# Kernel tuning notes

Measured on AMD Instinct MI355X. Metric: run time of the kernel, lower is better.

Reference implementation:

```python
import jax, jax.numpy as jnp
import numpy as np

K = 3       # kernel_size
STRIDE = 1
PAD = 1


def setup_inputs() -> dict:
    key = jax.random.key(0)
    k1, k2, k3 = jax.random.split(key, 3)
    B, C, H, W = 4, 64, 224, 224
    x = jax.random.normal(k1, (B, C, H, W), dtype=jnp.float32)
    # fc = Conv2d(C, C, 1) -> ReLU -> Conv2d(C, C*K*K, 1); 1x1 convs == per-pixel matmuls
    w1 = jax.random.normal(k2, (C, C), dtype=jnp.float32) * (1.0 / np.sqrt(C))
    w2 = jax.random.normal(k3, (C * K * K, C), dtype=jnp.float32) * (1.0 / np.sqrt(C))
    return {"x": x, "w1": w1, "w2": w2}


def reference(x, w1, w2):
    # Involution-style dynamic depthwise conv:
    # out[b,c,h,w] = sum_{i,j} kern[b,c,i,j,h,w] * x_pad[b,c,h+i,w+j]
    B, C, H, W = x.shape
    # kernel generator (two 1x1 convs with ReLU in between)
    h = jax.nn.relu(jnp.einsum('bchw,oc->bohw', x, w1))
    kern = jnp.einsum('bohw,po->bphw', h, w2).reshape(B, C, K * K, H, W)
    # unfold 3x3 neighborhoods (pad=1, stride=1) -> (B, C, K*K, H, W)
    xp = jnp.pad(x, ((0, 0), (0, 0), (PAD, PAD), (PAD, PAD)))
    patches = jnp.stack(
        [xp[:, :, i:i + H, j:j + W] for i in range(K) for j in range(K)], axis=2)
    return jnp.einsum('bckhw,bckhw->bchw', kern, patches)
```

## Files before the change

kernel.cpp:

```cpp
#include <hip/hip_runtime.h>

#define HH   224
#define WW   224
#define HW_  (HH * WW)
#define TS   16
#define TSH  18
#define NPIX (TSH * TSH)
#define XROW 144

typedef __attribute__((ext_vector_type(8))) short bf16x8;
typedef __attribute__((ext_vector_type(4))) short bf16x4;
typedef __attribute__((ext_vector_type(4))) float f32x4;

static __device__ __forceinline__ unsigned short f2bf(float f) {
    unsigned u = __float_as_uint(f);
    u += 0x7FFFu + ((u >> 16) & 1u);
    return (unsigned short)(u >> 16);
}
static __device__ __forceinline__ float bf2f(unsigned short h) {
    return __uint_as_float(((unsigned)h) << 16);
}

__global__ __launch_bounds__(256) void prep_weights(
    const float* __restrict__ w1, const float* __restrict__ w2,
    unsigned short* __restrict__ wsb)
{
    const int i = blockIdx.x * 256 + threadIdx.x;
    unsigned short* w1b = wsb;
    unsigned short* w2p = wsb + 4096;
    if (i < 4096) w1b[i] = f2bf(w1[i]);
    const int c  = i >> 10;
    const int rr = (i >> 6) & 15;
    const int o  = i & 63;
    float v = (rr < 9) ? w2[(c * 9 + rr) * 64 + o] : 0.f;
    w2p[i] = f2bf(v);
}

__global__ __launch_bounds__(256, 3) void dynconv_mfma16(
    const float* __restrict__ x, const unsigned short* __restrict__ wsb,
    float* __restrict__ out)
{
    __shared__ __align__(16) unsigned char xsb[NPIX * XROW];

    const unsigned char* w1b = (const unsigned char*)wsb;
    const unsigned char* w2p = (const unsigned char*)(wsb + 4096);

    const int b    = blockIdx.z;
    const int ty0  = blockIdx.y * TS;
    const int tx0  = blockIdx.x * TS;
    const int tid  = threadIdx.x;
    const int lane = tid & 63;
    const int w    = tid >> 6;
    const int tx   = lane & 15;
    const int g    = lane >> 4;

    const float* xb = x + (size_t)b * 64 * HW_;

    for (int i = tid; i < 32 * NPIX; i += 256) {
        int cp  = i / NPIX;
        int pix = i - cp * NPIX;
        int r   = pix / TSH;
        int col = pix - r * TSH;
        int gy  = ty0 + r - 1;
        int gx  = tx0 + col - 1;
        float f0 = 0.f, f1 = 0.f;
        if ((unsigned)gy < (unsigned)HH && (unsigned)gx < (unsigned)WW) {
            const float* p = xb + (size_t)(2 * cp) * HW_ + gy * WW + gx;
            f0 = p[0];
            f1 = p[HW_];
        }
        unsigned pk = (unsigned)f2bf(f0) | ((unsigned)f2bf(f1) << 16);
        *(unsigned*)(xsb + pix * XROW + cp * 4) = pk;
    }
    __syncthreads();

    bf16x4 bq[4][4];
    {
        bf16x8 aw1[4][2];
        #pragma unroll
        for (int mt = 0; mt < 4; ++mt)
            #pragma unroll
            for (int kt = 0; kt < 2; ++kt)
                aw1[mt][kt] = *(const bf16x8*)(w1b + (mt * 16 + tx) * 128 + kt * 64 + g * 16);
        #pragma unroll
        for (int q = 0; q < 4; ++q) {
            const int center = (w * 4 + q + 1) * TSH + (tx + 1);
            bf16x8 bx0 = *(const bf16x8*)(xsb + center * XROW + g * 16);
            bf16x8 bx1 = *(const bf16x8*)(xsb + center * XROW + 64 + g * 16);
            #pragma unroll
            for (int mt = 0; mt < 4; ++mt) {
                f32x4 hc = {0.f, 0.f, 0.f, 0.f};
                hc = __builtin_amdgcn_mfma_f32_16x16x32_bf16(aw1[mt][0], bx0, hc, 0, 0, 0);
                hc = __builtin_amdgcn_mfma_f32_16x16x32_bf16(aw1[mt][1], bx1, hc, 0, 0, 0);
                unsigned lo = (unsigned)f2bf(fmaxf(hc[0], 0.f)) | ((unsigned)f2bf(fmaxf(hc[1], 0.f)) << 16);
                unsigned hi = (unsigned)f2bf(fmaxf(hc[2], 0.f)) | ((unsigned)f2bf(fmaxf(hc[3], 0.f)) << 16);
                union { uint2 u; bf16x4 v; } cv;
                cv.u = make_uint2(lo, hi);
                bq[q][mt] = cv.v;
            }
        }
    }

    int poff[4][4];
    #pragma unroll
    for (int q = 0; q < 4; ++q)
        #pragma unroll
        for (int r = 0; r < 4; ++r) {
            int kk = g * 4 + r;
            int kv = kk < 9 ? kk : 0;
            int dy = kv / 3;
            int dx = kv - dy * 3;
            poff[q][r] = (w * 4 + q + dy) * TSH + (tx + dx);
        }

    float* outp = out + (size_t)b * 64 * HW_ + (size_t)(ty0 + w * 4 + g) * WW + tx0 + tx;

    const unsigned char* w2l = w2p + tx * 128 + g * 8;
    uint2 pf0[4], pf1[4];
    #pragma unroll
    for (int kb = 0; kb < 4; ++kb) {
        pf0[kb] = *(const uint2*)(w2l + kb * 32);
        pf1[kb] = *(const uint2*)(w2l + 2048 + kb * 32);
    }

    for (int c = 0; c < 64; c += 2) {
        union { uint2 u; bf16x4 v; } a2A[4], a2B[4];
        #pragma unroll
        for (int kb = 0; kb < 4; ++kb) { a2A[kb].u = pf0[kb]; a2B[kb].u = pf1[kb]; }
        const int cn = (c + 2 < 64) ? c + 2 : 62;
        #pragma unroll
        for (int kb = 0; kb < 4; ++kb) {
            pf0[kb] = *(const uint2*)(w2l + cn * 2048 + kb * 32);
            pf1[kb] = *(const uint2*)(w2l + (cn + 1) * 2048 + kb * 32);
        }

        f32x4 accA[4], accB[4];
        #pragma unroll
        for (int q = 0; q < 4; ++q) {
            accA[q] = f32x4{0.f, 0.f, 0.f, 0.f};
            accB[q] = f32x4{0.f, 0.f, 0.f, 0.f};
        }
        #pragma unroll
        for (int kb = 0; kb < 4; ++kb)
            #pragma unroll
            for (int q = 0; q < 4; ++q)
                accA[q] = __builtin_amdgcn_mfma_f32_16x16x16bf16_1k(a2A[kb].v, bq[q][kb], accA[q], 0, 0, 0);
        #pragma unroll
        for (int kb = 0; kb < 4; ++kb)
            #pragma unroll
            for (int q = 0; q < 4; ++q)
                accB[q] = __builtin_amdgcn_mfma_f32_16x16x16bf16_1k(a2B[kb].v, bq[q][kb], accB[q], 0, 0, 0);

        unsigned pp[4][4];
        #pragma unroll
        for (int q = 0; q < 4; ++q)
            #pragma unroll
            for (int r = 0; r < 4; ++r)
                pp[q][r] = *(const unsigned*)(xsb + poff[q][r] * XROW + c * 2);

        float pt[4], pu[4];
        #pragma unroll
        for (int q = 0; q < 4; ++q) {
            float s = 0.f, t = 0.f;
            #pragma unroll
            for (int r = 0; r < 4; ++r) {
                s = fmaf(accA[q][r], __uint_as_float(pp[q][r] << 16), s);
                t = fmaf(accB[q][r], __uint_as_float(pp[q][r] & 0xffff0000u), t);
            }
            s += __shfl_xor(s, 16, 64); s += __shfl_xor(s, 32, 64);
            t += __shfl_xor(t, 16, 64); t += __shfl_xor(t, 32, 64);
            pt[q] = s; pu[q] = t;
        }
        float vA = pt[0];
        vA = (g == 1) ? pt[1] : vA; vA = (g == 2) ? pt[2] : vA; vA = (g == 3) ? pt[3] : vA;
        float vB = pu[0];
        vB = (g == 1) ? pu[1] : vB; vB = (g == 2) ? pu[2] : vB; vB = (g == 3) ? pu[3] : vB;
        outp[(size_t)c * HW_] = vA;
        outp[(size_t)(c + 1) * HW_] = vB;
    }
}

extern "C" void kernel_launch(void* const* d_in, const int* in_sizes, int n_in,
                              void* d_out, int out_size, void* d_ws, size_t ws_size,
                              hipStream_t stream) {
    (void)in_sizes; (void)n_in; (void)out_size; (void)ws_size;
    const float* x  = (const float*)d_in[0];
    const float* w1 = (const float*)d_in[1];
    const float* w2 = (const float*)d_in[2];
    float* out = (float*)d_out;
    unsigned short* wsb = (unsigned short*)d_ws;

    prep_weights<<<256, 256, 0, stream>>>(w1, w2, wsb);

    dim3 grid(WW / TS, HH / TS, 4);
    dynconv_mfma16<<<grid, 256, 0, stream>>>(x, wsb, out);
}
```

Baseline: 248.1 us.

## Restructure dynamic conv as per-tap MFMA accumulation over all channels

```diff
diff --git a/kernel.cpp b/kernel.cpp
--- a/kernel.cpp
+++ b/kernel.cpp
@@ -4,9 +4,9 @@
 #define WW   224
 #define HW_  (HH * WW)
 #define TS   16
-#define TSH  18
-#define NPIX (TSH * TSH)
-#define XROW 144
+#define HL   18
+#define NPIX (HL * HL)
+#define XROW 136
 
 typedef __attribute__((ext_vector_type(8))) short bf16x8;
 typedef __attribute__((ext_vector_type(4))) short bf16x4;
@@ -25,25 +25,26 @@
     const float* __restrict__ w1, const float* __restrict__ w2,
     unsigned short* __restrict__ wsb)
 {
-    const int i = blockIdx.x * 256 + threadIdx.x;
+    const int j = blockIdx.x * 256 + threadIdx.x;
     unsigned short* w1b = wsb;
-    unsigned short* w2p = wsb + 4096;
-    if (i < 4096) w1b[i] = f2bf(w1[i]);
-    const int c  = i >> 10;
-    const int rr = (i >> 6) & 15;
-    const int o  = i & 63;
-    float v = (rr < 9) ? w2[(c * 9 + rr) * 64 + o] : 0.f;
-    w2p[i] = f2bf(v);
+    unsigned short* w2r = wsb + 4096;
+    if (j < 4096) w1b[j] = f2bf(w1[j]);
+    if (j < 36864) {
+        const int t = j >> 12;
+        const int c = (j >> 6) & 63;
+        const int o = j & 63;
+        w2r[j] = f2bf(w2[(c * 9 + t) * 64 + o]);
+    }
 }
 
-__global__ __launch_bounds__(256, 3) void dynconv_mfma16(
+__global__ __launch_bounds__(256, 3) void dynconv_tapacc(
     const float* __restrict__ x, const unsigned short* __restrict__ wsb,
     float* __restrict__ out)
 {
     __shared__ __align__(16) unsigned char xsb[NPIX * XROW];
 
-    const unsigned char* w1b = (const unsigned char*)wsb;
-    const unsigned char* w2p = (const unsigned char*)(wsb + 4096);
+    const unsigned char* w1b  = (const unsigned char*)wsb;
+    const unsigned char* w2rp = (const unsigned char*)(wsb + 4096);
 
     const int b    = blockIdx.z;
     const int ty0  = blockIdx.y * TS;
@@ -59,8 +60,8 @@
     for (int i = tid; i < 32 * NPIX; i += 256) {
         int cp  = i / NPIX;
         int pix = i - cp * NPIX;
-        int r   = pix / TSH;
-        int col = pix - r * TSH;
+        int r   = pix / HL;
+        int col = pix - r * HL;
         int gy  = ty0 + r - 1;
         int gx  = tx0 + col - 1;
         float f0 = 0.f, f1 = 0.f;
@@ -84,7 +85,7 @@
                 aw1[mt][kt] = *(const bf16x8*)(w1b + (mt * 16 + tx) * 128 + kt * 64 + g * 16);
         #pragma unroll
         for (int q = 0; q < 4; ++q) {
-            const int center = (w * 4 + q + 1) * TSH + (tx + 1);
+            const int center = (w * 4 + q + 1) * HL + (tx + 1);
             bf16x8 bx0 = *(const bf16x8*)(xsb + center * XROW + g * 16);
             bf16x8 bx1 = *(const bf16x8*)(xsb + center * XROW + 64 + g * 16);
             #pragma unroll
@@ -101,83 +102,56 @@
         }
     }
 
-    int poff[4][4];
+    f32x4 out_acc[4][4];
     #pragma unroll
     for (int q = 0; q < 4; ++q)
         #pragma unroll
-        for (int r = 0; r < 4; ++r) {
-            int kk = g * 4 + r;
-            int kv = kk < 9 ? kk : 0;
-            int dy = kv / 3;
-            int dx = kv - dy * 3;
-            poff[q][r] = (w * 4 + q + dy) * TSH + (tx + dx);
+        for (int m = 0; m < 4; ++m)
+            out_acc[q][m] = f32x4{0.f, 0.f, 0.f, 0.f};
+
+    const unsigned char* w2l = w2rp + tx * 128 + g * 8;
+
+    #pragma unroll
+    for (int t = 0; t < 9; ++t) {
+        const int dy = t / 3, dx = t - dy * 3;
+
+        union { uint2 u; bf16x4 v; } af[4][4];
+        #pragma unroll
+        for (int m = 0; m < 4; ++m)
+            #pragma unroll
+            for (int kb = 0; kb < 4; ++kb)
+                af[m][kb].u = *(const uint2*)(w2l + t * 8192 + m * 2048 + kb * 32);
+
+        int pby[4];
+        #pragma unroll
+        for (int q = 0; q < 4; ++q)
+            pby[q] = ((w * 4 + q + dy) * HL + (tx + dx)) * XROW + g * 8;
+
+        #pragma unroll
+        for (int m = 0; m < 4; ++m) {
+            #pragma unroll
+            for (int q = 0; q < 4; ++q) {
+                ushort4 pv = *(const ushort4*)(xsb + pby[q] + m * 32);
+                f32x4 kern = {0.f, 0.f, 0.f, 0.f};
+                #pragma unroll
+                for (int kb = 0; kb < 4; ++kb)
+                    kern = __builtin_amdgcn_mfma_f32_16x16x16bf16_1k(af[m][kb].v, bq[q][kb], kern, 0, 0, 0);
+                out_acc[q][m][0] = fmaf(kern[0], bf2f(pv.x), out_acc[q][m][0]);
+                out_acc[q][m][1] = fmaf(kern[1], bf2f(pv.y), out_acc[q][m][1]);
+                out_acc[q][m][2] = fmaf(kern[2], bf2f(pv.z), out_acc[q][m][2]);
+                out_acc[q][m][3] = fmaf(kern[3], bf2f(pv.w), out_acc[q][m][3]);
+            }
         }
-
-    float* outp = out + (size_t)b * 64 * HW_ + (size_t)(ty0 + w * 4 + g) * WW + tx0 + tx;
-
-    const unsigned char* w2l = w2p + tx * 128 + g * 8;
-    uint2 pf0[4], pf1[4];
-    #pragma unroll
-    for (int kb = 0; kb < 4; ++kb) {
-        pf0[kb] = *(const uint2*)(w2l + kb * 32);
-        pf1[kb] = *(const uint2*)(w2l + 2048 + kb * 32);
     }
 
-    for (int c = 0; c < 64; c += 2) {
-        union { uint2 u; bf16x4 v; } a2A[4], a2B[4];
-        #pragma unroll
-        for (int kb = 0; kb < 4; ++kb) { a2A[kb].u = pf0[kb]; a2B[kb].u = pf1[kb]; }
-        const int cn = (c + 2 < 64) ? c + 2 : 62;
-        #pragma unroll
-        for (int kb = 0; kb < 4; ++kb) {
-            pf0[kb] = *(const uint2*)(w2l + cn * 2048 + kb * 32);
-            pf1[kb] = *(const uint2*)(w2l + (cn + 1) * 2048 + kb * 32);
-        }
-
-        f32x4 accA[4], accB[4];
-        #pragma unroll
-        for (int q = 0; q < 4; ++q) {
-            accA[q] = f32x4{0.f, 0.f, 0.f, 0.f};
-            accB[q] = f32x4{0.f, 0.f, 0.f, 0.f};
-        }
-        #pragma unroll
-        for (int kb = 0; kb < 4; ++kb)
-            #pragma unroll
-            for (int q = 0; q < 4; ++q)
-                accA[q] = __builtin_amdgcn_mfma_f32_16x16x16bf16_1k(a2A[kb].v, bq[q][kb], accA[q], 0, 0, 0);
-        #pragma unroll
-        for (int kb = 0; kb < 4; ++kb)
-            #pragma unroll
-            for (int q = 0; q < 4; ++q)
-                accB[q] = __builtin_amdgcn_mfma_f32_16x16x16bf16_1k(a2B[kb].v, bq[q][kb], accB[q], 0, 0, 0);
-
-        unsigned pp[4][4];
+    float* ob = out + (size_t)b * 64 * HW_ + (size_t)(ty0 + w * 4) * WW + tx0 + tx;
+    #pragma unroll
+    for (int m = 0; m < 4; ++m)
         #pragma unroll
         for (int q = 0; q < 4; ++q)
             #pragma unroll
             for (int r = 0; r < 4; ++r)
-                pp[q][r] = *(const unsigned*)(xsb + poff[q][r] * XROW + c * 2);
-
-        float pt[4], pu[4];
-        #pragma unroll
-        for (int q = 0; q < 4; ++q) {
-            float s = 0.f, t = 0.f;
-            #pragma unroll
-            for (int r = 0; r < 4; ++r) {
-                s = fmaf(accA[q][r], __uint_as_float(pp[q][r] << 16), s);
-                t = fmaf(accB[q][r], __uint_as_float(pp[q][r] & 0xffff0000u), t);
-            }
-            s += __shfl_xor(s, 16, 64); s += __shfl_xor(s, 32, 64);
-            t += __shfl_xor(t, 16, 64); t += __shfl_xor(t, 32, 64);
-            pt[q] = s; pu[q] = t;
-        }
-        float vA = pt[0];
-        vA = (g == 1) ? pt[1] : vA; vA = (g == 2) ? pt[2] : vA; vA = (g == 3) ? pt[3] : vA;
-        float vB = pu[0];
-        vB = (g == 1) ? pu[1] : vB; vB = (g == 2) ? pu[2] : vB; vB = (g == 3) ? pu[3] : vB;
-        outp[(size_t)c * HW_] = vA;
-        outp[(size_t)(c + 1) * HW_] = vB;
-    }
+                ob[(size_t)(m * 16 + 4 * g + r) * HW_ + q * WW] = out_acc[q][m][r];
 }
 
 extern "C" void kernel_launch(void* const* d_in, const int* in_sizes, int n_in,
@@ -190,8 +164,8 @@
     float* out = (float*)d_out;
     unsigned short* wsb = (unsigned short*)d_ws;
 
-    prep_weights<<<256, 256, 0, stream>>>(w1, w2, wsb);
+    prep_weights<<<144, 256, 0, stream>>>(w1, w2, wsb);
 
     dim3 grid(WW / TS, HH / TS, 4);
-    dynconv_mfma16<<<grid, 256, 0, stream>>>(x, wsb, out);
+    dynconv_tapacc<<<grid, 256, 0, stream>>>(x, wsb, out);
 }
```

Result: slower. 327.9 us (+32.2%).
